# Performance work log

Hardware: AMD Instinct MI355X
Metric: run time of the kernel (lower is better)

## Reference

```python
import jax, jax.numpy as jnp
import numpy as np

N = 20000      # nodes
E = 320000     # edges (before self-loops)
IN = 128       # in_features
H = 8          # heads
C = 120        # out channels per head
SLOPE = 0.2    # LeakyReLU negative slope (PyG default)


def setup_inputs() -> dict:
    key = jax.random.key(0)
    k = jax.random.split(key, 8)
    x = jax.random.normal(k[0], (N, IN), jnp.float32)
    edge_index = jax.random.randint(k[1], (2, E), 0, N)  # [2,E], row0=src, row1=dst
    W = jax.random.normal(k[2], (IN, H * C), jnp.float32) / np.sqrt(IN)
    att_src = jax.random.normal(k[3], (H, C), jnp.float32) * 0.1
    att_dst = jax.random.normal(k[4], (H, C), jnp.float32) * 0.1
    bias = jnp.zeros((H * C,), jnp.float32)
    fc_w = jax.random.normal(k[5], (H * C, 2), jnp.float32) / np.sqrt(H * C)
    fc_b = jnp.zeros((2,), jnp.float32)
    return dict(x=x, edge_index=edge_index, W=W, att_src=att_src,
                att_dst=att_dst, bias=bias, fc_w=fc_w, fc_b=fc_b)


def reference(x, edge_index, W, att_src, att_dst, bias, fc_w, fc_b):
    n = x.shape[0]
    # add self loops (GATConv default add_self_loops=True)
    loops = jnp.arange(n, dtype=edge_index.dtype)
    ei = jnp.concatenate([edge_index, jnp.stack([loops, loops])], axis=1)
    src, dst = ei[0], ei[1]
    # per-head linear projection: [n, H, C]
    xp = (x @ W).reshape(n, H, C)
    # per-node attention logits
    a_s = jnp.einsum('nhc,hc->nh', xp, att_src)  # [n,H]
    a_d = jnp.einsum('nhc,hc->nh', xp, att_dst)  # [n,H]
    # edge-wise logits + LeakyReLU: [Etot,H]
    e = jax.nn.leaky_relu(a_s[src] + a_d[dst], SLOPE)
    # segment softmax over incoming edges of each destination node
    emax = jax.lax.stop_gradient(jax.ops.segment_max(e, dst, num_segments=n))
    ee = jnp.exp(e - emax[dst])
    denom = jax.ops.segment_sum(ee, dst, num_segments=n)
    alpha = ee / denom[dst]                      # [Etot,H]
    # scatter-aggregate weighted messages: [n,H,C]
    out = jax.ops.segment_sum(alpha[:, :, None] * xp[src], dst, num_segments=n)
    out = out.reshape(n, H * C) + bias           # concat heads + bias
    return out @ fc_w + fc_b                     # final Linear -> [n,2]
```

## Files before the change

kernel.cpp:

```cpp
#include <hip/hip_runtime.h>

#define NN    20000
#define EDGES 320000
#define HH    8
#define CC    120
#define HC    960
#define SLOPE 0.2f
#define BUCKET 64
#define NB    128
#define CH    (EDGES / NB)
#define NQ    (NN / 4)


__global__ __launch_bounds__(256) void prep_kernel(const float* __restrict__ W,
                                                   const float* __restrict__ att_src,
                                                   const float* __restrict__ att_dst,
                                                   const float* __restrict__ bias,
                                                   const float* __restrict__ fc_w,
                                                   const float* __restrict__ fc_b,
                                                   const int* __restrict__ ei,
                                                   float* __restrict__ U,
                                                   float* __restrict__ cbias,
                                                   unsigned* __restrict__ hist,
                                                   unsigned char* __restrict__ rank) {
  __shared__ unsigned hsh[NQ];
  int t = threadIdx.x, b = blockIdx.x;
  int l = t & 63;
  if (b < NB) {
    for (int i = t; i < NQ; i += 256) hsh[i] = 0u;
    __syncthreads();
    const int* dsts = ei + EDGES + b * CH;
    unsigned char* rnk = rank + b * CH;
    for (int i = t; i < CH; i += 256) {
      int d = dsts[i];
      unsigned sh = (d & 3) * 8;
      unsigned old = atomicAdd(&hsh[d >> 2], 1u << sh);
      rnk[i] = (unsigned char)(old >> sh);
    }
    __syncthreads();
    unsigned* hrow = hist + (size_t)b * NQ;
    for (int i = t; i < NQ; i += 256) hrow[i] = hsh[i];
  } else if (b < 384) {
    int p = (b - 128) * 4 + (t >> 6);
    int k = p >> 3, h = p & 7;
    const float* wrow = W + (size_t)k * HC + h * CC;
    const float* asv  = att_src + h * CC;
    const float* adv  = att_dst + h * CC;
    const float2* fv  = (const float2*)fc_w + h * CC;
    bool tail = (l < CC - 64);
    float w0 = wrow[l],            w1 = tail ? wrow[64 + l] : 0.f;
    float s0 = asv[l],             s1 = tail ? asv[64 + l] : 0.f;
    float d0 = adv[l],             d1 = tail ? adv[64 + l] : 0.f;
    float2 f0 = fv[l];
    float2 f1 = tail ? fv[64 + l] : make_float2(0.f, 0.f);
    float a_s = w0 * s0 + w1 * s1;
    float a_d = w0 * d0 + w1 * d1;
    float z0  = w0 * f0.x + w1 * f1.x;
    float z1  = w0 * f0.y + w1 * f1.y;
#pragma unroll
    for (int m = 1; m < 64; m <<= 1) {
      a_s += __shfl_xor(a_s, m);
      a_d += __shfl_xor(a_d, m);
      z0  += __shfl_xor(z0, m);
      z1  += __shfl_xor(z1, m);
    }
    if (l == 0) {
      float* u = U + k * 32 + 4 * h;
      u[0] = a_s; u[1] = z0; u[2] = z1; u[3] = a_d;
    }
  } else if (t < 128) {
    int j = t >> 6;
    float acc = 0.f;
    for (int m = l; m < HC; m += 64) acc = fmaf(bias[m], fc_w[m * 2 + j], acc);
#pragma unroll
    for (int m = 1; m < 64; m <<= 1) acc += __shfl_xor(acc, m);
    if (l == 0) cbias[j] = acc + fc_b[j];
  }
}

__global__ __launch_bounds__(256) void scan_kernel(const unsigned* __restrict__ hist,
                                                   unsigned* __restrict__ base,
                                                   uint4* __restrict__ deg4) {
  int j = blockIdx.x * 256 + threadIdx.x;
  if (j >= NQ) return;
  unsigned s0 = 0, s1 = 0, s2 = 0, s3 = 0;
#pragma unroll 8
  for (int c = 0; c < NB; ++c) {
    unsigned v = hist[(size_t)c * NQ + j];
    base[(size_t)c * NQ + j] = s0 | (s1 << 8) | (s2 << 16) | (s3 << 24);
    s0 += v & 0xFFu;
    s1 += (v >> 8) & 0xFFu;
    s2 += (v >> 16) & 0xFFu;
    s3 += (v >> 24) & 0xFFu;
  }
  deg4[j] = make_uint4(s0, s1, s2, s3);
}

__global__ __launch_bounds__(128) void projplace_kernel(const float* __restrict__ x,
                                                        const float* __restrict__ U,
                                                        const int* __restrict__ ei,
                                                        const unsigned* __restrict__ base,
                                                        const unsigned char* __restrict__ rank,
                                                        unsigned* __restrict__ list,
                                                        float* __restrict__ P) {
  int t = threadIdx.x;
  int b = blockIdx.x;

  if (b >= 625) {
    int e0 = (b - 625) * 256 + t;
#pragma unroll
    for (int j = 0; j < 2; ++j) {
      int e = e0 + j * 128;
      int d = ei[EDGES + e];
      unsigned r = rank[e];
      unsigned c = (unsigned)e / (unsigned)CH;
      unsigned packed = base[(size_t)c * NQ + (d >> 2)];
      unsigned bs = (packed >> ((d & 3) * 8)) & 0xFFu;
      list[(size_t)d * BUCKET + bs + r] = (unsigned)ei[e];
    }
    return;
  }

  __shared__ float Us[128 * 32];
  int n0 = b * 32;
  const float4* U4 = (const float4*)U;
#pragma unroll
  for (int j = 0; j < 8; ++j) ((float4*)Us)[t + j * 128] = U4[t + j * 128];
  __syncthreads();

  int rq = t >> 3, cq = t & 7;
  const float4* xr0 = (const float4*)(x + (size_t)(n0 + rq) * 128);
  const float4* xr1 = (const float4*)(x + (size_t)(n0 + rq + 16) * 128);
  float a00 = 0.f, a01 = 0.f, a02 = 0.f, a03 = 0.f;
  float a10 = 0.f, a11 = 0.f, a12 = 0.f, a13 = 0.f;
#pragma unroll 4
  for (int k4 = 0; k4 < 32; ++k4) {
    float4 xa = xr0[k4];
    float4 xb = xr1[k4];
    float4 u0 = *(const float4*)(Us + (k4 * 4 + 0) * 32 + 4 * cq);
    float4 u1 = *(const float4*)(Us + (k4 * 4 + 1) * 32 + 4 * cq);
    float4 u2 = *(const float4*)(Us + (k4 * 4 + 2) * 32 + 4 * cq);
    float4 u3 = *(const float4*)(Us + (k4 * 4 + 3) * 32 + 4 * cq);
    a00 = fmaf(xa.x, u0.x, a00); a01 = fmaf(xa.x, u0.y, a01);
    a02 = fmaf(xa.x, u0.z, a02); a03 = fmaf(xa.x, u0.w, a03);
    a10 = fmaf(xb.x, u0.x, a10); a11 = fmaf(xb.x, u0.y, a11);
    a12 = fmaf(xb.x, u0.z, a12); a13 = fmaf(xb.x, u0.w, a13);
    a00 = fmaf(xa.y, u1.x, a00); a01 = fmaf(xa.y, u1.y, a01);
    a02 = fmaf(xa.y, u1.z, a02); a03 = fmaf(xa.y, u1.w, a03);
    a10 = fmaf(xb.y, u1.x, a10); a11 = fmaf(xb.y, u1.y, a11);
    a12 = fmaf(xb.y, u1.z, a12); a13 = fmaf(xb.y, u1.w, a13);
    a00 = fmaf(xa.z, u2.x, a00); a01 = fmaf(xa.z, u2.y, a01);
    a02 = fmaf(xa.z, u2.z, a02); a03 = fmaf(xa.z, u2.w, a03);
    a10 = fmaf(xb.z, u2.x, a10); a11 = fmaf(xb.z, u2.y, a11);
    a12 = fmaf(xb.z, u2.z, a12); a13 = fmaf(xb.z, u2.w, a13);
    a00 = fmaf(xa.w, u3.x, a00); a01 = fmaf(xa.w, u3.y, a01);
    a02 = fmaf(xa.w, u3.z, a02); a03 = fmaf(xa.w, u3.w, a03);
    a10 = fmaf(xb.w, u3.x, a10); a11 = fmaf(xb.w, u3.y, a11);
    a12 = fmaf(xb.w, u3.z, a12); a13 = fmaf(xb.w, u3.w, a13);
  }
  *(float4*)(P + (size_t)(n0 + rq) * 32 + 4 * cq) =
      make_float4(a00, a01, a02, a03);
  *(float4*)(P + (size_t)(n0 + rq + 16) * 32 + 4 * cq) =
      make_float4(a10, a11, a12, a13);
}

__global__ __launch_bounds__(256) void gather_kernel(const unsigned* __restrict__ deg_,
                                                     const unsigned* __restrict__ list,
                                                     const float* __restrict__ P,
                                                     const float* __restrict__ cbias,
                                                     float* __restrict__ out) {
  int t = threadIdx.x;
  int wave = t >> 6;
  int lane = t & 63;
  int h = lane & 7;
  int o = lane >> 3;
  int dst = blockIdx.x * 4 + wave;

  const float* pd = P + (size_t)dst * 32;
  float4 pd4 = *(const float4*)(pd + 4 * h);
  float ad = pd4.w;
  unsigned deg = deg_[dst];
  unsigned rv = list[(size_t)dst * BUCKET + lane];

  float accd = 0.f, acc0 = 0.f, acc1 = 0.f;
  if (o == 0) {
    float v = pd4.x + ad;
    v = (v > 0.f) ? v : SLOPE * v;
    float ex = __expf(v);
    accd = ex;
    acc0 = ex * pd4.y;
    acc1 = ex * pd4.z;
  }

  {
    unsigned e0 = o, e1 = o + 8;
    unsigned s0 = __shfl(rv, (int)e0);
    unsigned s1 = __shfl(rv, (int)e1);
    bool m0 = e0 < deg, m1 = e1 < deg;
    unsigned a0 = m0 ? s0 : (unsigned)dst;
    unsigned a1 = m1 ? s1 : (unsigned)dst;
    float4 q0 = *(const float4*)(P + (size_t)a0 * 32 + 4 * h);
    float4 q1 = *(const float4*)(P + (size_t)a1 * 32 + 4 * h);
    if (m0) {
      float v = q0.x + ad; v = (v > 0.f) ? v : SLOPE * v;
      float ex = __expf(v);
      accd += ex; acc0 = fmaf(ex, q0.y, acc0); acc1 = fmaf(ex, q0.z, acc1);
    }
    if (m1) {
      float v = q1.x + ad; v = (v > 0.f) ? v : SLOPE * v;
      float ex = __expf(v);
      accd += ex; acc0 = fmaf(ex, q1.y, acc0); acc1 = fmaf(ex, q1.z, acc1);
    }
  }
  if (deg > 16u) {
    unsigned e2 = o + 16, e3 = o + 24;
    unsigned s2 = __shfl(rv, (int)e2);
    unsigned s3 = __shfl(rv, (int)e3);
    bool m2 = e2 < deg, m3 = e3 < deg;
    unsigned a2 = m2 ? s2 : (unsigned)dst;
    unsigned a3 = m3 ? s3 : (unsigned)dst;
    float4 q2 = *(const float4*)(P + (size_t)a2 * 32 + 4 * h);
    float4 q3 = *(const float4*)(P + (size_t)a3 * 32 + 4 * h);
    if (m2) {
      float v = q2.x + ad; v = (v > 0.f) ? v : SLOPE * v;
      float ex = __expf(v);
      accd += ex; acc0 = fmaf(ex, q2.y, acc0); acc1 = fmaf(ex, q2.z, acc1);
    }
    if (m3) {
      float v = q3.x + ad; v = (v > 0.f) ? v : SLOPE * v;
      float ex = __expf(v);
      accd += ex; acc0 = fmaf(ex, q3.y, acc0); acc1 = fmaf(ex, q3.z, acc1);
    }
  }
  if (deg > 32u) {
    unsigned iters = (deg - 32u + 7u) >> 3;
    unsigned e = 32u + (unsigned)o;
    for (unsigned i = 0; i < iters; ++i, e += 8u) {
      unsigned src = __shfl(rv, (int)e);
      if (e < deg) {
        float4 q = *(const float4*)(P + (size_t)src * 32 + 4 * h);
        float v = q.x + ad; v = (v > 0.f) ? v : SLOPE * v;
        float ex = __expf(v);
        accd += ex; acc0 = fmaf(ex, q.y, acc0); acc1 = fmaf(ex, q.z, acc1);
      }
    }
  }
  float accd_tot = accd + __shfl_xor(accd, 8);
  accd_tot += __shfl_xor(accd_tot, 16);
  accd_tot += __shfl_xor(accd_tot, 32);
  float rcp = 1.0f / accd_tot;
  float r0 = acc0 * rcp;
  float r1 = acc1 * rcp;
#pragma unroll
  for (int m = 1; m < 64; m <<= 1) {
    r0 += __shfl_xor(r0, m);
    r1 += __shfl_xor(r1, m);
  }
  if (lane == 0) {
    ((float2*)out)[dst] = make_float2(cbias[0] + r0, cbias[1] + r1);
  }
}

extern "C" void kernel_launch(void* const* d_in, const int* in_sizes, int n_in,
                              void* d_out, int out_size, void* d_ws, size_t ws_size,
                              hipStream_t stream) {
  const float* x       = (const float*)d_in[0];
  const int*   ei      = (const int*)d_in[1];
  const float* W       = (const float*)d_in[2];
  const float* att_src = (const float*)d_in[3];
  const float* att_dst = (const float*)d_in[4];
  const float* bias    = (const float*)d_in[5];
  const float* fc_w    = (const float*)d_in[6];
  const float* fc_b    = (const float*)d_in[7];
  float* out = (float*)d_out;

  float*    U     = (float*)d_ws;
  float*    cbias = U + 4096;
  float*    P     = U + 8192;
  unsigned* deg   = (unsigned*)(P + (size_t)NN * 32);
  unsigned* list  = deg + NN;
  unsigned* hist  = list + (size_t)NN * BUCKET;
  unsigned* base  = hist + (size_t)NB * NQ;
  unsigned char* rank = (unsigned char*)(base + (size_t)NB * NQ);

  prep_kernel<<<385, 256, 0, stream>>>(W, att_src, att_dst, bias, fc_w, fc_b,
                                       ei, U, cbias, hist, rank);
  scan_kernel<<<20, 256, 0, stream>>>(hist, base, (uint4*)deg);
  projplace_kernel<<<1875, 128, 0, stream>>>(x, U, ei, base, rank, list, P);
  gather_kernel<<<NN / 4, 256, 0, stream>>>(deg, list, P, cbias, out);
}
```

Before: 45.80 us.

## Stage x tiles in LDS for projection, reorder prep blocks, unconditionally issue gather loads

The projection blocks now cover 64 nodes each and stage the x tile in padded shared memory, so each thread computes four rows from LDS instead of two rows from direct global loads. The grid drops from 1875 to 1563 blocks. In prep_kernel the block roles are reordered so the U and cbias work comes first and the histogram blocks come after. The gather kernel always issues the first four neighbor loads without the deg>16 branch, which raises memory-level parallelism at the cost of redundant self loads for low-degree nodes. A larger LDS footprint may lower occupancy.

```diff
diff --git a/kernel.cpp b/kernel.cpp
--- a/kernel.cpp
+++ b/kernel.cpp
@@ -26,22 +26,8 @@
   __shared__ unsigned hsh[NQ];
   int t = threadIdx.x, b = blockIdx.x;
   int l = t & 63;
-  if (b < NB) {
-    for (int i = t; i < NQ; i += 256) hsh[i] = 0u;
-    __syncthreads();
-    const int* dsts = ei + EDGES + b * CH;
-    unsigned char* rnk = rank + b * CH;
-    for (int i = t; i < CH; i += 256) {
-      int d = dsts[i];
-      unsigned sh = (d & 3) * 8;
-      unsigned old = atomicAdd(&hsh[d >> 2], 1u << sh);
-      rnk[i] = (unsigned char)(old >> sh);
-    }
-    __syncthreads();
-    unsigned* hrow = hist + (size_t)b * NQ;
-    for (int i = t; i < NQ; i += 256) hrow[i] = hsh[i];
-  } else if (b < 384) {
-    int p = (b - 128) * 4 + (t >> 6);
+  if (b < 256) {
+    int p = b * 4 + (t >> 6);
     int k = p >> 3, h = p & 7;
     const float* wrow = W + (size_t)k * HC + h * CC;
     const float* asv  = att_src + h * CC;
@@ -68,13 +54,30 @@
       float* u = U + k * 32 + 4 * h;
       u[0] = a_s; u[1] = z0; u[2] = z1; u[3] = a_d;
     }
-  } else if (t < 128) {
-    int j = t >> 6;
-    float acc = 0.f;
-    for (int m = l; m < HC; m += 64) acc = fmaf(bias[m], fc_w[m * 2 + j], acc);
-#pragma unroll
-    for (int m = 1; m < 64; m <<= 1) acc += __shfl_xor(acc, m);
-    if (l == 0) cbias[j] = acc + fc_b[j];
+  } else if (b == 256) {
+    if (t < 128) {
+      int j = t >> 6;
+      float acc = 0.f;
+      for (int m = l; m < HC; m += 64) acc = fmaf(bias[m], fc_w[m * 2 + j], acc);
+#pragma unroll
+      for (int m = 1; m < 64; m <<= 1) acc += __shfl_xor(acc, m);
+      if (l == 0) cbias[j] = acc + fc_b[j];
+    }
+  } else {
+    int c = b - 257;
+    for (int i = t; i < NQ; i += 256) hsh[i] = 0u;
+    __syncthreads();
+    const int* dsts = ei + EDGES + c * CH;
+    unsigned char* rnk = rank + c * CH;
+    for (int i = t; i < CH; i += 256) {
+      int d = dsts[i];
+      unsigned sh = (d & 3) * 8;
+      unsigned old = atomicAdd(&hsh[d >> 2], 1u << sh);
+      rnk[i] = (unsigned char)((old >> sh) & 0xFFu);
+    }
+    __syncthreads();
+    unsigned* hrow = hist + (size_t)c * NQ;
+    for (int i = t; i < NQ; i += 256) hrow[i] = hsh[i];
   }
 }
 
@@ -96,6 +99,7 @@
   deg4[j] = make_uint4(s0, s1, s2, s3);
 }
 
+#define XSTR 132
 __global__ __launch_bounds__(128) void projplace_kernel(const float* __restrict__ x,
                                                         const float* __restrict__ U,
                                                         const int* __restrict__ ei,
@@ -106,8 +110,8 @@
   int t = threadIdx.x;
   int b = blockIdx.x;
 
-  if (b >= 625) {
-    int e0 = (b - 625) * 256 + t;
+  if (b >= 313) {
+    int e0 = (b - 313) * 256 + t;
 #pragma unroll
     for (int j = 0; j < 2; ++j) {
       int e = e0 + j * 128;
@@ -121,47 +125,58 @@
     return;
   }
 
+  __shared__ float xs[64 * XSTR];
   __shared__ float Us[128 * 32];
-  int n0 = b * 32;
+  int n0 = b * 64;
+  const float4* xg = (const float4*)(x + (size_t)n0 * 128);
   const float4* U4 = (const float4*)U;
 #pragma unroll
   for (int j = 0; j < 8; ++j) ((float4*)Us)[t + j * 128] = U4[t + j * 128];
+#pragma unroll
+  for (int j = 0; j < 16; ++j) {
+    int i = t + j * 128;
+    int row = i >> 5, q = i & 31;
+    if (n0 + row < NN) *(float4*)(xs + row * XSTR + q * 4) = xg[i];
+  }
   __syncthreads();
 
   int rq = t >> 3, cq = t & 7;
-  const float4* xr0 = (const float4*)(x + (size_t)(n0 + rq) * 128);
-  const float4* xr1 = (const float4*)(x + (size_t)(n0 + rq + 16) * 128);
-  float a00 = 0.f, a01 = 0.f, a02 = 0.f, a03 = 0.f;
-  float a10 = 0.f, a11 = 0.f, a12 = 0.f, a13 = 0.f;
-#pragma unroll 4
+  float4 acc[4];
+#pragma unroll
+  for (int rr = 0; rr < 4; ++rr) acc[rr] = make_float4(0.f, 0.f, 0.f, 0.f);
+#pragma unroll 2
   for (int k4 = 0; k4 < 32; ++k4) {
-    float4 xa = xr0[k4];
-    float4 xb = xr1[k4];
     float4 u0 = *(const float4*)(Us + (k4 * 4 + 0) * 32 + 4 * cq);
     float4 u1 = *(const float4*)(Us + (k4 * 4 + 1) * 32 + 4 * cq);
     float4 u2 = *(const float4*)(Us + (k4 * 4 + 2) * 32 + 4 * cq);
     float4 u3 = *(const float4*)(Us + (k4 * 4 + 3) * 32 + 4 * cq);
-    a00 = fmaf(xa.x, u0.x, a00); a01 = fmaf(xa.x, u0.y, a01);
-    a02 = fmaf(xa.x, u0.z, a02); a03 = fmaf(xa.x, u0.w, a03);
-    a10 = fmaf(xb.x, u0.x, a10); a11 = fmaf(xb.x, u0.y, a11);
-    a12 = fmaf(xb.x, u0.z, a12); a13 = fmaf(xb.x, u0.w, a13);
-    a00 = fmaf(xa.y, u1.x, a00); a01 = fmaf(xa.y, u1.y, a01);
-    a02 = fmaf(xa.y, u1.z, a02); a03 = fmaf(xa.y, u1.w, a03);
-    a10 = fmaf(xb.y, u1.x, a10); a11 = fmaf(xb.y, u1.y, a11);
-    a12 = fmaf(xb.y, u1.z, a12); a13 = fmaf(xb.y, u1.w, a13);
-    a00 = fmaf(xa.z, u2.x, a00); a01 = fmaf(xa.z, u2.y, a01);
-    a02 = fmaf(xa.z, u2.z, a02); a03 = fmaf(xa.z, u2.w, a03);
-    a10 = fmaf(xb.z, u2.x, a10); a11 = fmaf(xb.z, u2.y, a11);
-    a12 = fmaf(xb.z, u2.z, a12); a13 = fmaf(xb.z, u2.w, a13);
-    a00 = fmaf(xa.w, u3.x, a00); a01 = fmaf(xa.w, u3.y, a01);
-    a02 = fmaf(xa.w, u3.z, a02); a03 = fmaf(xa.w, u3.w, a03);
-    a10 = fmaf(xb.w, u3.x, a10); a11 = fmaf(xb.w, u3.y, a11);
-    a12 = fmaf(xb.w, u3.z, a12); a13 = fmaf(xb.w, u3.w, a13);
-  }
-  *(float4*)(P + (size_t)(n0 + rq) * 32 + 4 * cq) =
-      make_float4(a00, a01, a02, a03);
-  *(float4*)(P + (size_t)(n0 + rq + 16) * 32 + 4 * cq) =
-      make_float4(a10, a11, a12, a13);
+#pragma unroll
+    for (int rr = 0; rr < 4; ++rr) {
+      float4 xa = *(const float4*)(xs + (rq + rr * 16) * XSTR + k4 * 4);
+      acc[rr].x = fmaf(xa.x, u0.x, acc[rr].x);
+      acc[rr].y = fmaf(xa.x, u0.y, acc[rr].y);
+      acc[rr].z = fmaf(xa.x, u0.z, acc[rr].z);
+      acc[rr].w = fmaf(xa.x, u0.w, acc[rr].w);
+      acc[rr].x = fmaf(xa.y, u1.x, acc[rr].x);
+      acc[rr].y = fmaf(xa.y, u1.y, acc[rr].y);
+      acc[rr].z = fmaf(xa.y, u1.z, acc[rr].z);
+      acc[rr].w = fmaf(xa.y, u1.w, acc[rr].w);
+      acc[rr].x = fmaf(xa.z, u2.x, acc[rr].x);
+      acc[rr].y = fmaf(xa.z, u2.y, acc[rr].y);
+      acc[rr].z = fmaf(xa.z, u2.z, acc[rr].z);
+      acc[rr].w = fmaf(xa.z, u2.w, acc[rr].w);
+      acc[rr].x = fmaf(xa.w, u3.x, acc[rr].x);
+      acc[rr].y = fmaf(xa.w, u3.y, acc[rr].y);
+      acc[rr].z = fmaf(xa.w, u3.z, acc[rr].z);
+      acc[rr].w = fmaf(xa.w, u3.w, acc[rr].w);
+    }
+  }
+#pragma unroll
+  for (int rr = 0; rr < 4; ++rr) {
+    int row = n0 + rq + rr * 16;
+    if (row < NN)
+      *(float4*)(P + (size_t)row * 32 + 4 * cq) = acc[rr];
+  }
 }
 
 __global__ __launch_bounds__(256) void gather_kernel(const unsigned* __restrict__ deg_,
@@ -192,45 +207,39 @@
     acc1 = ex * pd4.z;
   }
 
-  {
-    unsigned e0 = o, e1 = o + 8;
-    unsigned s0 = __shfl(rv, (int)e0);
-    unsigned s1 = __shfl(rv, (int)e1);
-    bool m0 = e0 < deg, m1 = e1 < deg;
-    unsigned a0 = m0 ? s0 : (unsigned)dst;
-    unsigned a1 = m1 ? s1 : (unsigned)dst;
-    float4 q0 = *(const float4*)(P + (size_t)a0 * 32 + 4 * h);
-    float4 q1 = *(const float4*)(P + (size_t)a1 * 32 + 4 * h);
-    if (m0) {
-      float v = q0.x + ad; v = (v > 0.f) ? v : SLOPE * v;
-      float ex = __expf(v);
-      accd += ex; acc0 = fmaf(ex, q0.y, acc0); acc1 = fmaf(ex, q0.z, acc1);
-    }
-    if (m1) {
-      float v = q1.x + ad; v = (v > 0.f) ? v : SLOPE * v;
-      float ex = __expf(v);
-      accd += ex; acc0 = fmaf(ex, q1.y, acc0); acc1 = fmaf(ex, q1.z, acc1);
-    }
-  }
-  if (deg > 16u) {
-    unsigned e2 = o + 16, e3 = o + 24;
-    unsigned s2 = __shfl(rv, (int)e2);
-    unsigned s3 = __shfl(rv, (int)e3);
-    bool m2 = e2 < deg, m3 = e3 < deg;
-    unsigned a2 = m2 ? s2 : (unsigned)dst;
-    unsigned a3 = m3 ? s3 : (unsigned)dst;
-    float4 q2 = *(const float4*)(P + (size_t)a2 * 32 + 4 * h);
-    float4 q3 = *(const float4*)(P + (size_t)a3 * 32 + 4 * h);
-    if (m2) {
-      float v = q2.x + ad; v = (v > 0.f) ? v : SLOPE * v;
-      float ex = __expf(v);
-      accd += ex; acc0 = fmaf(ex, q2.y, acc0); acc1 = fmaf(ex, q2.z, acc1);
-    }
-    if (m3) {
-      float v = q3.x + ad; v = (v > 0.f) ? v : SLOPE * v;
-      float ex = __expf(v);
-      accd += ex; acc0 = fmaf(ex, q3.y, acc0); acc1 = fmaf(ex, q3.z, acc1);
-    }
+  unsigned e0 = o, e1 = o + 8, e2 = o + 16, e3 = o + 24;
+  unsigned s0 = __shfl(rv, (int)e0);
+  unsigned s1 = __shfl(rv, (int)e1);
+  unsigned s2 = __shfl(rv, (int)e2);
+  unsigned s3 = __shfl(rv, (int)e3);
+  bool m0 = e0 < deg, m1 = e1 < deg, m2 = e2 < deg, m3 = e3 < deg;
+  unsigned a0 = m0 ? s0 : (unsigned)dst;
+  unsigned a1 = m1 ? s1 : (unsigned)dst;
+  unsigned a2 = m2 ? s2 : (unsigned)dst;
+  unsigned a3 = m3 ? s3 : (unsigned)dst;
+  float4 q0 = *(const float4*)(P + (size_t)a0 * 32 + 4 * h);
+  float4 q1 = *(const float4*)(P + (size_t)a1 * 32 + 4 * h);
+  float4 q2 = *(const float4*)(P + (size_t)a2 * 32 + 4 * h);
+  float4 q3 = *(const float4*)(P + (size_t)a3 * 32 + 4 * h);
+  if (m0) {
+    float v = q0.x + ad; v = (v > 0.f) ? v : SLOPE * v;
+    float ex = __expf(v);
+    accd += ex; acc0 = fmaf(ex, q0.y, acc0); acc1 = fmaf(ex, q0.z, acc1);
+  }
+  if (m1) {
+    float v = q1.x + ad; v = (v > 0.f) ? v : SLOPE * v;
+    float ex = __expf(v);
+    accd += ex; acc0 = fmaf(ex, q1.y, acc0); acc1 = fmaf(ex, q1.z, acc1);
+  }
+  if (m2) {
+    float v = q2.x + ad; v = (v > 0.f) ? v : SLOPE * v;
+    float ex = __expf(v);
+    accd += ex; acc0 = fmaf(ex, q2.y, acc0); acc1 = fmaf(ex, q2.z, acc1);
+  }
+  if (m3) {
+    float v = q3.x + ad; v = (v > 0.f) ? v : SLOPE * v;
+    float ex = __expf(v);
+    accd += ex; acc0 = fmaf(ex, q3.y, acc0); acc1 = fmaf(ex, q3.z, acc1);
   }
   if (deg > 32u) {
     unsigned iters = (deg - 32u + 7u) >> 3;
@@ -286,6 +295,6 @@
   prep_kernel<<<385, 256, 0, stream>>>(W, att_src, att_dst, bias, fc_w, fc_b,
                                        ei, U, cbias, hist, rank);
   scan_kernel<<<20, 256, 0, stream>>>(hist, base, (uint4*)deg);
-  projplace_kernel<<<1875, 128, 0, stream>>>(x, U, ei, base, rank, list, P);
+  projplace_kernel<<<1563, 128, 0, stream>>>(x, U, ei, base, rank, list, P);
   gather_kernel<<<NN / 4, 256, 0, stream>>>(deg, list, P, cbias, out);
 }
```

Measured after the change: 50.09 us. 9.4% more time.
